# Kernel tuning notes

Hardware: AMD Instinct MI355X
Metric: run time of the kernel (lower is better)

The kernel has to match this reference:

```python
import jax, jax.numpy as jnp
import numpy as np
import math

B, S, C, H = 32, 500, 1024, 16
D = C // H  # head dim = 64

def setup_inputs() -> dict:
    key = jax.random.key(0)
    ks = jax.random.split(key, 9)
    sc = 1.0 / math.sqrt(C)
    return {
        "x": jax.random.normal(ks[0], (B, S, C), dtype=jnp.float32),
        "Wq": jax.random.normal(ks[1], (C, C), dtype=jnp.float32) * sc,
        "bq": jnp.zeros((C,), dtype=jnp.float32),
        "Wk": jax.random.normal(ks[2], (C, C), dtype=jnp.float32) * sc,
        "bk": jnp.zeros((C,), dtype=jnp.float32),
        "Wv": jax.random.normal(ks[3], (C, C), dtype=jnp.float32) * sc,
        "bv": jnp.zeros((C,), dtype=jnp.float32),
        "Wp": jax.random.normal(ks[4], (C, C), dtype=jnp.float32) * sc,
        "bp": jnp.zeros((C,), dtype=jnp.float32),
    }

def reference(x, Wq, bq, Wk, bk, Wv, bv, Wp, bp):
    # Projections -> [B, H, S, D]
    q = (x @ Wq + bq).reshape(B, S, H, D).transpose(0, 2, 1, 3)
    k = (x @ Wk + bk).reshape(B, S, H, D).transpose(0, 2, 1, 3)
    v = (x @ Wv + bv).reshape(B, S, H, D).transpose(0, 2, 1, 3)
    # Scaled scores [B, H, S, S]
    att = jnp.einsum('bhqd,bhkd->bhqk', q, k) * (1.0 / math.sqrt(D))
    causal = jnp.tril(jnp.ones((S, S), dtype=bool))
    att = jnp.where(causal[None, None], att, jnp.float32(-1e10))
    att = jax.nn.softmax(att, axis=-1)
    # (dropout is identity in eval mode)
    y = jnp.einsum('bhqk,bhkd->bhqd', att, v)  # [B, H, S, D]
    y = y.transpose(0, 2, 1, 3).reshape(B, S, C)
    return y @ Wp + bp
```

## Files before the change

kernel.cpp:

```cpp
#include <hip/hip_runtime.h>
#include <math.h>

#define B_ 32
#define S_ 500
#define C_ 1024
#define H_ 16
#define D_ 64
#define M_ (B_ * S_)
#define MP 16128
#define SP 512

typedef _Float16 f16;
typedef f16 f16x8 __attribute__((ext_vector_type(8)));
typedef f16 f16x4 __attribute__((ext_vector_type(4)));
typedef float f32x4 __attribute__((ext_vector_type(4)));

#define GLOBAL_AS __attribute__((address_space(1)))
#define LDS_AS __attribute__((address_space(3)))

__device__ __forceinline__ void async_load16(const void* g, void* l) {
    __builtin_amdgcn_global_load_lds((const GLOBAL_AS void*)g, (LDS_AS void*)l, 16, 0, 0);
}
template <int N>
__device__ __forceinline__ void wait_vmcnt() {
    asm volatile("s_waitcnt vmcnt(%0)" ::"i"(N) : "memory");
}

struct MaskF { static constexpr bool value = false; };
struct MaskT { static constexpr bool value = true; };

__global__ __launch_bounds__(256) void prep(
    const float* __restrict__ x, f16* __restrict__ xf, int n8_real, int n8_tot,
    const float* __restrict__ W0, const float* __restrict__ W1,
    const float* __restrict__ W2, const float* __restrict__ W3,
    f16* __restrict__ T0, f16* __restrict__ T1,
    f16* __restrict__ T2, f16* __restrict__ T3)
{
    __shared__ float t[32][33];
    const int bid = blockIdx.x;
    const int tid = threadIdx.x;
    if (bid < 4096) {
        const int z = bid >> 10, rem = bid & 1023;
        const float* W = (z == 0) ? W0 : (z == 1) ? W1 : (z == 2) ? W2 : W3;
        f16* T = (z == 0) ? T0 : (z == 1) ? T1 : (z == 2) ? T2 : T3;
        const int n0 = (rem & 31) * 32, k0 = (rem >> 5) * 32;
        const int tx = tid & 31, ty = tid >> 5;
#pragma unroll
        for (int i = 0; i < 4; ++i)
            t[ty + 8 * i][tx] = W[(size_t)(k0 + ty + 8 * i) * C_ + n0 + tx];
        __syncthreads();
#pragma unroll
        for (int i = 0; i < 4; ++i) {
            int n = ty + 8 * i;
            T[(size_t)(n0 + n) * C_ + k0 + tx] = (f16)t[tx][n];
        }
    } else {
        int i = (bid - 4096) * 256 + tid;
        if (i >= n8_tot) return;
        f16x8 h;
        if (i < n8_real) {
            float4 a = ((const float4*)x)[2 * i];
            float4 b = ((const float4*)x)[2 * i + 1];
            h[0] = (f16)a.x; h[1] = (f16)a.y; h[2] = (f16)a.z; h[3] = (f16)a.w;
            h[4] = (f16)b.x; h[5] = (f16)b.y; h[6] = (f16)b.z; h[7] = (f16)b.w;
        } else {
            f16 z8 = (f16)0.f;
            h[0] = z8; h[1] = z8; h[2] = z8; h[3] = z8;
            h[4] = z8; h[5] = z8; h[6] = z8; h[7] = z8;
        }
        ((f16x8*)xf)[i] = h;
    }
}

#define BAR()                          \
    __builtin_amdgcn_s_barrier();      \
    __builtin_amdgcn_sched_barrier(0)

#define LD_A(MH)                                                              \
    _Pragma("unroll") for (int i = 0; i < 4; ++i)                             \
    _Pragma("unroll") for (int ks = 0; ks < 2; ++ks)                          \
        af[i][ks] = *(const f16x8*)(smem + c * 32768 + rowA +                 \
                                    ((MH) * 64 + i * 16) * 64 + sw[ks]);

#define LD_B(NH)                                                              \
    _Pragma("unroll") for (int j = 0; j < 2; ++j)                             \
    _Pragma("unroll") for (int ks = 0; ks < 2; ++ks)                          \
        bf[NH][j][ks] = *(const f16x8*)(smem + c * 32768 + rowB +             \
                                        ((NH) * 32 + j * 16) * 64 + sw[ks]);

#define MMA(MH, NH)                                                           \
    __builtin_amdgcn_s_setprio(1);                                            \
    _Pragma("unroll") for (int i = 0; i < 4; ++i)                             \
    _Pragma("unroll") for (int j = 0; j < 2; ++j)                             \
    _Pragma("unroll") for (int ks = 0; ks < 2; ++ks)                          \
        acc[(MH) * 4 + i][(NH) * 2 + j] =                                     \
            __builtin_amdgcn_mfma_f32_16x16x32_f16(                           \
                af[i][ks], bf[NH][j][ks], acc[(MH) * 4 + i][(NH) * 2 + j],    \
                0, 0, 0);                                                     \
    __builtin_amdgcn_s_setprio(0)

template <int MODE>
__global__ __launch_bounds__(512) void gemm256(
    const f16* __restrict__ A, const f16* __restrict__ W,
    const float* __restrict__ b0, const float* __restrict__ b1,
    const float* __restrict__ b2, void* __restrict__ o0,
    void* __restrict__ o1, void* __restrict__ o2)
{
    constexpr int K = C_;
    constexpr int NB = (MODE == 0) ? 12 : 4;
    constexpr int NWG = 63 * NB;
    constexpr int Q8 = NWG / 8, R8 = NWG % 8;
    extern __shared__ __align__(16) f16 smem[];

    const int tid = threadIdx.x;
    const int lane = tid & 63, w = tid >> 6;
    const int wm = w >> 2, wn = w & 3;
    const int quad = lane >> 4, lr = lane & 15;

    const int lin = blockIdx.x;
    const int xcd = lin & 7, pos = lin >> 3;
    const int wg = (xcd < R8 ? xcd * (Q8 + 1) : R8 * (Q8 + 1) + (xcd - R8) * Q8) + pos;
    const int m0 = (wg / NB) * 256;
    const int n0 = (wg % NB) * 256;

    const int srow = tid >> 3, sj = tid & 7;
    const int gc = sj ^ (srow & 7);
    const f16* pA = A + (size_t)(m0 + srow) * K + gc * 8;
    const f16* pB = W + (size_t)(n0 + srow) * K + gc * 8;
    f16* dA = smem + tid * 8;
    f16* dB = smem + 16384 + tid * 8;

    auto stageA = [&](int kt, int cb, int h) __attribute__((always_inline)) {
        const f16* s = pA + (size_t)(h * 128) * K + kt * 64;
        f16* d = dA + cb * 32768 + h * 8192;
        async_load16(s, d);
        async_load16(s + (size_t)64 * K, d + 4096);
    };
    auto stageB = [&](int kt, int cb, int h) __attribute__((always_inline)) {
        const f16* s = pB + (size_t)(h * 128) * K + kt * 64;
        f16* d = dB + cb * 32768 + h * 8192;
        async_load16(s, d);
        async_load16(s + (size_t)64 * K, d + 4096);
    };

    int sw[2];
    sw[0] = ((0 + quad) ^ (lr & 7)) * 8;
    sw[1] = ((4 + quad) ^ (lr & 7)) * 8;
    const int rowA = (wm * 128 + lr) * 64;
    const int rowB = 16384 + (wn * 64 + lr) * 64;

    f32x4 acc[8][4];
#pragma unroll
    for (int i = 0; i < 8; ++i)
#pragma unroll
        for (int j = 0; j < 4; ++j) acc[i][j] = (f32x4)0.f;
    f16x8 af[4][2], bf[2][2][2];

    stageA(0, 0, 0); stageA(0, 0, 1); stageB(0, 0, 0); stageB(0, 0, 1);

    constexpr int NT = K / 64;
    for (int kt = 0; kt < NT; ++kt) {
        const int c = kt & 1;
        BAR();
        if (kt + 1 < NT) {
            stageA(kt + 1, c ^ 1, 0); stageA(kt + 1, c ^ 1, 1);
            stageB(kt + 1, c ^ 1, 0); stageB(kt + 1, c ^ 1, 1);
            wait_vmcnt<8>();
        } else {
            wait_vmcnt<0>();
        }
        BAR();
        LD_A(0); LD_B(0);
        MMA(0, 0);
        LD_B(1);
        MMA(0, 1);
        LD_A(1);
        MMA(1, 1);
        MMA(1, 0);
    }

#pragma unroll
    for (int nf = 0; nf < 4; ++nf) {
        int gcn = n0 + wn * 64 + nf * 16 + lr;
        if (MODE == 1) {
            float bv = b0[gcn];
            float* of = (float*)o0;
#pragma unroll
            for (int mf = 0; mf < 8; ++mf) {
                int gr0 = m0 + wm * 128 + mf * 16 + quad * 4;
                if (gr0 >= M_) continue;
#pragma unroll
                for (int r = 0; r < 4; ++r)
                    of[(size_t)(gr0 + r) * C_ + gcn] = acc[mf][nf][r] + bv;
            }
        } else {
            int sec = gcn >> 10;
            int gcl = gcn & 1023;
            const float* bp = (sec == 0) ? b0 : (sec == 1) ? b1 : b2;
            float bv = bp[gcl];
            float osc = (sec == 0) ? 0.125f : 1.0f;
            int h = gcl >> 6, d = gcl & 63;
#pragma unroll
            for (int mf = 0; mf < 8; ++mf) {
                int gr0 = m0 + wm * 128 + mf * 16 + quad * 4;
                if (gr0 >= M_) continue;
                int b = gr0 / S_, s0 = gr0 - b * S_;
                if (sec < 2) {
                    f16* oq = (f16*)((sec == 0) ? o0 : o1);
#pragma unroll
                    for (int r = 0; r < 4; ++r) {
                        float v = (acc[mf][nf][r] + bv) * osc;
                        size_t idx = (((size_t)b * H_ + h) * S_ + (s0 + r)) * D_ + d;
                        oq[idx] = (f16)v;
                    }
                } else {
                    f16* ov = (f16*)o2;
                    f16x4 pk;
#pragma unroll
                    for (int r = 0; r < 4; ++r) pk[r] = (f16)(acc[mf][nf][r] + bv);
                    *(f16x4*)(ov + (((size_t)b * H_ + h) * D_ + d) * SP + s0) = pk;
                }
            }
        }
    }
}

__global__ __launch_bounds__(256) void attn_mfma(
    const f16* __restrict__ qg, const f16* __restrict__ kg,
    const f16* __restrict__ vt, f16* __restrict__ Y)
{
    __shared__ __align__(16) f16 sK[64 * 64];
    __shared__ __align__(16) f16 sVt[64 * 64];
    __shared__ __align__(16) f16 sP[4 * 32 * 64];

    const int tid = threadIdx.x;
    const int lin = blockIdx.x;
    const int xcd = lin & 7;
    const int pos = lin >> 3;
    const int bh = xcd * 64 + (pos >> 2);
    const int qt = 3 - (pos & 3);
    const int q0 = qt * 128;
    const int lane = tid & 63, w = tid >> 6;
    const int quad = lane >> 4, lr = lane & 15;
    const size_t gbase = (size_t)bh * S_ * D_;
    const size_t vbase = (size_t)bh * D_ * SP;
    const int psw = (lr & 7) << 1;

    f16x8 qf[2][2];
#pragma unroll
    for (int t = 0; t < 2; ++t) {
        int q = q0 + w * 32 + t * 16 + lr;
        const f16* pq = qg + gbase + (size_t)q * D_;
#pragma unroll
        for (int s2 = 0; s2 < 2; ++s2)
            qf[t][s2] = *(const f16x8*)(pq + quad * 8 + 32 * s2);
    }

    f32x4 accO[2][4];
#pragma unroll
    for (int t = 0; t < 2; ++t)
#pragma unroll
        for (int nt = 0; nt < 4; ++nt) accO[t][nt] = (f32x4)0.f;
    float l_run[2] = {0.f, 0.f};

    auto iter = [&](int kt, auto masked_tag) __attribute__((always_inline)) {
        constexpr bool MASKED = decltype(masked_tag)::value;
        const int k0 = kt * 64;
#pragma unroll
        for (int it = 0; it < 2; ++it) {
            int idx = it * 256 + tid;
            int row = idx >> 3, c = idx & 7;
            int csw = (c ^ (row & 7)) * 8;
            async_load16(kg + gbase + (size_t)(k0 + row) * D_ + csw, &sK[idx * 8]);
            async_load16(vt + vbase + (size_t)row * SP + k0 + csw, &sVt[idx * 8]);
        }
        __syncthreads();

        f32x4 accS[4][2];
#pragma unroll
        for (int mt = 0; mt < 4; ++mt)
#pragma unroll
            for (int t = 0; t < 2; ++t) accS[mt][t] = (f32x4)0.f;
        __builtin_amdgcn_s_setprio(1);
#pragma unroll
        for (int mt = 0; mt < 4; ++mt) {
            int row = mt * 16 + lr;
#pragma unroll
            for (int s2 = 0; s2 < 2; ++s2) {
                int off = row * 64 + (((quad + 4 * s2) ^ (lr & 7)) << 3);
                f16x8 ka = *(const f16x8*)&sK[off];
#pragma unroll
                for (int t = 0; t < 2; ++t)
                    accS[mt][t] = __builtin_amdgcn_mfma_f32_16x16x32_f16(
                        ka, qf[t][s2], accS[mt][t], 0, 0, 0);
            }
        }
        __builtin_amdgcn_s_setprio(0);

        float ls[2] = {0.f, 0.f};
#pragma unroll
        for (int mt = 0; mt < 4; ++mt)
#pragma unroll
            for (int t = 0; t < 2; ++t) {
                f16x4 pk;
#pragma unroll
                for (int r = 0; r < 4; ++r) {
                    float s = accS[mt][t][r];
                    if (MASKED) {
                        int key = k0 + mt * 16 + quad * 4 + r;
                        int qq = q0 + w * 32 + t * 16 + lr;
                        s = (key <= qq && key < S_) ? s : -1e30f;
                    }
                    float p = __expf(s);
                    ls[t] += p;
                    pk[r] = (f16)p;
                }
                int c8 = (mt * 4 + quad) ^ psw;
                *(f16x4*)&sP[w * 2048 + (t * 16 + lr) * 64 + c8 * 4] = pk;
            }
        ls[0] += __shfl_xor(ls[0], 16); ls[0] += __shfl_xor(ls[0], 32);
        ls[1] += __shfl_xor(ls[1], 16); ls[1] += __shfl_xor(ls[1], 32);
        l_run[0] += ls[0];
        l_run[1] += ls[1];

        __builtin_amdgcn_s_setprio(1);
#pragma unroll
        for (int t = 0; t < 2; ++t) {
            int pb = w * 2048 + (t * 16 + lr) * 64;
#pragma unroll
            for (int s2 = 0; s2 < 2; ++s2) {
                int c8 = (quad * 2 + 8 * s2) ^ psw;
                f16x8 pf = *(const f16x8*)&sP[pb + c8 * 4];
#pragma unroll
                for (int nt = 0; nt < 4; ++nt) {
                    f16x8 vf = *(const f16x8*)
                        &sVt[(nt * 16 + lr) * 64 + (((quad + 4 * s2) ^ (lr & 7)) << 3)];
                    accO[t][nt] = __builtin_amdgcn_mfma_f32_16x16x32_f16(
                        pf, vf, accO[t][nt], 0, 0, 0);
                }
            }
        }
        __builtin_amdgcn_s_setprio(0);
        __syncthreads();
    };

    for (int kt = 0; kt < 2 * qt; ++kt) iter(kt, MaskF{});
    iter(2 * qt, MaskT{});
    iter(2 * qt + 1, MaskT{});

    const int b = bh >> 4, h = bh & 15;
#pragma unroll
    for (int t = 0; t < 2; ++t) {
#pragma unroll
        for (int r = 0; r < 4; ++r) {
            float lsum = __shfl(l_run[t], quad * 4 + r);
            float iv = 1.f / lsum;
            int s = q0 + w * 32 + t * 16 + quad * 4 + r;
            if (s >= S_) continue;
            size_t rowbase = (size_t)(b * S_ + s) * C_ + h * 64;
#pragma unroll
            for (int nt = 0; nt < 4; ++nt)
                Y[rowbase + nt * 16 + lr] = (f16)(accO[t][nt][r] * iv);
        }
    }
}

extern "C" void kernel_launch(void* const* d_in, const int* in_sizes, int n_in,
                              void* d_out, int out_size, void* d_ws, size_t ws_size,
                              hipStream_t stream)
{
    const float* x = (const float*)d_in[0];
    const float* Wq = (const float*)d_in[1];
    const float* bq = (const float*)d_in[2];
    const float* Wk = (const float*)d_in[3];
    const float* bk = (const float*)d_in[4];
    const float* Wv = (const float*)d_in[5];
    const float* bv = (const float*)d_in[6];
    const float* Wp = (const float*)d_in[7];
    const float* bp = (const float*)d_in[8];

    const size_t NEL = (size_t)M_ * C_;
    const size_t WEL = (size_t)C_ * C_;
    f16* qf = (f16*)d_ws;
    f16* kf = qf + NEL;
    f16* vtw = kf + NEL;
    f16* xf = vtw + (size_t)B_ * H_ * D_ * SP;
    f16* wpf = xf + (size_t)MP * C_;
    f16* yf = xf;

    f16* wq = (f16*)d_out;
    f16* wk = wq + WEL;
    f16* wv = wk + WEL;

    hipFuncSetAttribute(reinterpret_cast<const void*>(&gemm256<0>),
                        hipFuncAttributeMaxDynamicSharedMemorySize, 131072);
    hipFuncSetAttribute(reinterpret_cast<const void*>(&gemm256<1>),
                        hipFuncAttributeMaxDynamicSharedMemorySize, 131072);

    int n8r = (int)(NEL / 8);
    int n8t = (int)((size_t)MP * C_ / 8);
    int nprep = 4096 + (n8t + 255) / 256;
    prep<<<nprep, 256, 0, stream>>>(x, xf, n8r, n8t,
                                    Wq, Wk, Wv, Wp, wq, wk, wv, wpf);

    gemm256<0><<<756, 512, 131072, stream>>>(xf, wq, bq, bk, bv, qf, kf, vtw);

    attn_mfma<<<2048, 256, 0, stream>>>(qf, kf, vtw, yf);

    gemm256<1><<<252, 512, 131072, stream>>>(yf, wpf, bp, nullptr, nullptr,
                                             d_out, nullptr, nullptr);
}
```

Before: 368.6 us.

## Split GEMM tile loads into quarter-stages interleaved with MFMA phases

Reorganizes the LDS layout so each half-tile of A and B (by warp row/column group) sits in a contiguous 8192-element region. The main loop then issues the next k-tile's loads in four pieces, each interleaved with one MMA sub-phase, and waits with finer vmcnt counts. This replaces the two full barriers per iteration with per-quarter barriers, and peels the final iteration out of the loop. The aim is to overlap global-to-LDS traffic with compute rather than stalling at the top of each iteration. The cost is more barriers and tighter ordering constraints on the double buffer.

```diff
diff --git a/kernel.cpp b/kernel.cpp
--- a/kernel.cpp
+++ b/kernel.cpp
@@ -79,14 +79,15 @@
 #define LD_A(MH)                                                              \
     _Pragma("unroll") for (int i = 0; i < 4; ++i)                             \
     _Pragma("unroll") for (int ks = 0; ks < 2; ++ks)                          \
-        af[i][ks] = *(const f16x8*)(smem + c * 32768 + rowA +                 \
-                                    ((MH) * 64 + i * 16) * 64 + sw[ks]);
+        af[i][ks] = *(const f16x8*)(smem + c * 32768 + (MH) * 8192 +          \
+                                    rA_off + i * 1024 + sw[ks]);
 
 #define LD_B(NH)                                                              \
     _Pragma("unroll") for (int j = 0; j < 2; ++j)                             \
     _Pragma("unroll") for (int ks = 0; ks < 2; ++ks)                          \
-        bf[NH][j][ks] = *(const f16x8*)(smem + c * 32768 + rowB +             \
-                                        ((NH) * 32 + j * 16) * 64 + sw[ks]);
+        bf[NH][j][ks] = *(const f16x8*)(smem + c * 32768 + 16384 +            \
+                                        (NH) * 8192 + rB_off + j * 1024 +     \
+                                        sw[ks]);
 
 #define MMA(MH, NH)                                                           \
     __builtin_amdgcn_s_setprio(1);                                            \
@@ -123,31 +124,31 @@
     const int m0 = (wg / NB) * 256;
     const int n0 = (wg % NB) * 256;
 
-    const int srow = tid >> 3, sj = tid & 7;
-    const int gc = sj ^ (srow & 7);
-    const f16* pA = A + (size_t)(m0 + srow) * K + gc * 8;
-    const f16* pB = W + (size_t)(n0 + srow) * K + gc * 8;
+    const int srow = tid >> 3;
+    const int gc8 = (tid & 7) ^ (srow & 7);
+    const f16* pAt = A + (size_t)(m0 + srow) * K + gc8 * 8;
+    const f16* pBt = W + (size_t)(n0 + (srow & 31) + ((srow >> 5) << 6)) * K + gc8 * 8;
     f16* dA = smem + tid * 8;
     f16* dB = smem + 16384 + tid * 8;
 
     auto stageA = [&](int kt, int cb, int h) __attribute__((always_inline)) {
-        const f16* s = pA + (size_t)(h * 128) * K + kt * 64;
+        const f16* s = pAt + (size_t)(h * 64) * K + kt * 64;
         f16* d = dA + cb * 32768 + h * 8192;
         async_load16(s, d);
-        async_load16(s + (size_t)64 * K, d + 4096);
+        async_load16(s + (size_t)128 * K, d + 4096);
     };
     auto stageB = [&](int kt, int cb, int h) __attribute__((always_inline)) {
-        const f16* s = pB + (size_t)(h * 128) * K + kt * 64;
+        const f16* s = pBt + (size_t)(h * 32) * K + kt * 64;
         f16* d = dB + cb * 32768 + h * 8192;
         async_load16(s, d);
-        async_load16(s + (size_t)64 * K, d + 4096);
+        async_load16(s + (size_t)128 * K, d + 4096);
     };
 
     int sw[2];
     sw[0] = ((0 + quad) ^ (lr & 7)) * 8;
     sw[1] = ((4 + quad) ^ (lr & 7)) * 8;
-    const int rowA = (wm * 128 + lr) * 64;
-    const int rowB = 16384 + (wn * 64 + lr) * 64;
+    const int rA_off = (wm * 64 + lr) * 64;
+    const int rB_off = (wn * 32 + lr) * 64;
 
     f32x4 acc[8][4];
 #pragma unroll
@@ -156,24 +157,35 @@
         for (int j = 0; j < 4; ++j) acc[i][j] = (f32x4)0.f;
     f16x8 af[4][2], bf[2][2][2];
 
-    stageA(0, 0, 0); stageA(0, 0, 1); stageB(0, 0, 0); stageB(0, 0, 1);
+    stageA(0, 0, 0); stageB(0, 0, 0); stageB(0, 0, 1); stageA(0, 0, 1);
 
     constexpr int NT = K / 64;
-    for (int kt = 0; kt < NT; ++kt) {
-        const int c = kt & 1;
-        BAR();
-        if (kt + 1 < NT) {
-            stageA(kt + 1, c ^ 1, 0); stageA(kt + 1, c ^ 1, 1);
-            stageB(kt + 1, c ^ 1, 0); stageB(kt + 1, c ^ 1, 1);
-            wait_vmcnt<8>();
-        } else {
-            wait_vmcnt<0>();
-        }
-        BAR();
+    for (int kt = 0; kt < NT - 1; ++kt) {
+        const int c = kt & 1, nb = c ^ 1;
+        stageA(kt + 1, nb, 0);
+        wait_vmcnt<6>(); BAR();
         LD_A(0); LD_B(0);
         MMA(0, 0);
+        stageB(kt + 1, nb, 0);
+        wait_vmcnt<6>(); BAR();
         LD_B(1);
         MMA(0, 1);
+        stageB(kt + 1, nb, 1);
+        wait_vmcnt<6>(); BAR();
+        LD_A(1);
+        MMA(1, 1);
+        stageA(kt + 1, nb, 1);
+        MMA(1, 0);
+    }
+    {
+        const int c = (NT - 1) & 1;
+        wait_vmcnt<4>(); BAR();
+        LD_A(0); LD_B(0);
+        MMA(0, 0);
+        wait_vmcnt<2>(); BAR();
+        LD_B(1);
+        MMA(0, 1);
+        wait_vmcnt<0>(); BAR();
         LD_A(1);
         MMA(1, 1);
         MMA(1, 0);
```

New measurement: 363.9 us. No clear change (-1.3%).
